# Kernel tuning notes

Hardware: AMD Instinct MI355X
Metric: run time of the kernel (lower is better)

The kernel has to match this reference:

```python
import jax, jax.numpy as jnp
import numpy as np

N_SITES = 100000
DIM = 128
KSIZE = 7  # 7^3 = 343 offsets
GRID = 160


def _build_sparse_structure(seed=0):
    """Sample N_SITES unique voxels in a GRID^3 volume and build the
    depthwise-conv kernel map: neighbor_idx[i, k] = index of site at
    coords[i] + offset[k], or N_SITES (sentinel -> zero row) if absent."""
    rng = np.random.default_rng(seed)
    lin = rng.choice(GRID ** 3, size=N_SITES, replace=False)
    coords = np.stack(np.unravel_index(lin, (GRID, GRID, GRID)), axis=1).astype(np.int64)  # [N,3]
    lookup = np.full(GRID ** 3, N_SITES, dtype=np.int32)
    lookup[lin] = np.arange(N_SITES, dtype=np.int32)
    r = KSIZE // 2
    offs = np.stack(np.meshgrid(*([np.arange(-r, r + 1)] * 3), indexing="ij"), axis=-1).reshape(-1, 3)  # [343,3]
    K = offs.shape[0]
    neighbor_idx = np.full((N_SITES, K), N_SITES, dtype=np.int32)
    for k in range(K):
        nb = coords + offs[k]
        ok = np.all((nb >= 0) & (nb < GRID), axis=1)
        nb_lin = (nb[ok, 0] * GRID + nb[ok, 1]) * GRID + nb[ok, 2]
        neighbor_idx[ok, k] = lookup[nb_lin]
    return neighbor_idx


def setup_inputs() -> dict:
    key = jax.random.key(0)
    ks = jax.random.split(key, 12)
    neighbor_idx = jnp.asarray(_build_sparse_structure(0))
    d, h = DIM, 4 * DIM
    K = KSIZE ** 3
    return {
        "feats": jax.random.normal(ks[0], (N_SITES, d), jnp.float32),
        "neighbor_idx": neighbor_idx,
        "dw_w": jax.random.normal(ks[1], (K, d), jnp.float32) * 0.05,
        "dw_b": jax.random.normal(ks[2], (d,), jnp.float32) * 0.02,
        "ln_g": 1.0 + 0.1 * jax.random.normal(ks[3], (d,), jnp.float32),
        "ln_b": 0.02 * jax.random.normal(ks[4], (d,), jnp.float32),
        "w1": jax.random.normal(ks[5], (d, h), jnp.float32) * (1.0 / np.sqrt(d)),
        "b1": 0.02 * jax.random.normal(ks[6], (h,), jnp.float32),
        "grn_g": 0.1 * jax.random.normal(ks[7], (1, h), jnp.float32),
        "grn_b": 0.02 * jax.random.normal(ks[8], (1, h), jnp.float32),
        "w2": jax.random.normal(ks[9], (h, d), jnp.float32) * (1.0 / np.sqrt(h)),
        "b2": 0.02 * jax.random.normal(ks[10], (d,), jnp.float32),
    }


def reference(feats, neighbor_idx, dw_w, dw_b, ln_g, ln_b, w1, b1, grn_g, grn_b, w2, b2):
    eps = 1e-6
    n, d = feats.shape
    # --- sparse depthwise conv: gather-multiply-accumulate over kernel offsets ---
    f_pad = jnp.concatenate([feats, jnp.zeros((1, d), feats.dtype)], axis=0)  # sentinel row

    def step(acc, xs):
        idx_k, w_k = xs  # idx_k: [N], w_k: [dim]
        return acc + f_pad[idx_k] * w_k, None

    x, _ = jax.lax.scan(step, jnp.zeros_like(feats), (neighbor_idx.T, dw_w))
    x = x + dw_b
    # --- LayerNorm over channels ---
    mu = jnp.mean(x, axis=-1, keepdims=True)
    var = jnp.var(x, axis=-1, keepdims=True)
    x = (x - mu) / jnp.sqrt(var + eps) * ln_g + ln_b
    # --- pwconv1 -> GELU (exact, matching torch default) ---
    x = jax.nn.gelu(x @ w1 + b1, approximate=False)  # [N, 4*dim]
    # --- GRN: L2 norm over all sites (dim=0), per channel ---
    gx = jnp.sqrt(jnp.sum(x * x, axis=0, keepdims=True))  # [1, 4*dim]
    nx = gx / (jnp.mean(gx, axis=-1, keepdims=True) + eps)
    x = grn_g * (x * nx) + grn_b + x
    # --- pwconv2 + residual (drop_path identity in eval) ---
    x = x @ w2 + b2
    return feats + x
```

## Files before the change

### kernel.cpp

```cpp
#include <hip/hip_runtime.h>

typedef unsigned short u16;
typedef unsigned int u32;
typedef __attribute__((ext_vector_type(8))) short bf16x8;
typedef __attribute__((ext_vector_type(4))) float f32x4;

__device__ __forceinline__ u16 f2bf(float f) {
    u32 u = __float_as_uint(f);
    return (u16)((u + 0x7FFFu + ((u >> 16) & 1u)) >> 16);
}

__device__ __forceinline__ float fast_gelu(float x) {
    const float x3 = x * x * x;
    const float y2 = 1.5957691216057308f * (x + 0.044715f * x3);
    const float u = __expf(fminf(y2, 80.f));
    const float th = (u - 1.f) / (u + 1.f);
    return 0.5f * x * (1.f + th);
}

__global__ __launch_bounds__(256) void cast_feats_k(
    const float* __restrict__ src, u16* __restrict__ dst, int n4)
{
    const int e = blockIdx.x * 256 + threadIdx.x;
    if (e >= n4) return;
    const float4 v = *(const float4*)(src + (size_t)e * 4);
    uint2 o;
    o.x = (u32)f2bf(v.x) | ((u32)f2bf(v.y) << 16);
    o.y = (u32)f2bf(v.z) | ((u32)f2bf(v.w) << 16);
    *(uint2*)(dst + (size_t)e * 4) = o;
}

__global__ __launch_bounds__(256) void dwln_k(
    const u16* __restrict__ featsb, const int* __restrict__ nb,
    const u16* __restrict__ dwwb, const float* __restrict__ dw_b,
    const float* __restrict__ ln_g, const float* __restrict__ ln_b,
    u16* __restrict__ xln, int nsites)
{
    __shared__ int lists[8][348];
    const int w = threadIdx.x >> 6;
    const int lane = threadIdx.x & 63;
    const int s0 = blockIdx.x * 8 + w * 2;
    if (s0 >= nsites) return;
    const bool two = (s0 + 1) < nsites;
    const int* rowA = nb + (size_t)s0 * 343;
    const int* rowB = nb + (size_t)(two ? s0 + 1 : s0) * 343;
    int idxA[6], idxB[6];
    #pragma unroll
    for (int j = 0; j < 5; ++j) {
        idxA[j] = rowA[lane + j * 64];
        const int vb = rowB[lane + j * 64];
        idxB[j] = two ? vb : nsites;
    }
    idxA[5] = (lane < 23) ? rowA[320 + lane] : nsites;
    idxB[5] = (two && lane < 23) ? rowB[320 + lane] : nsites;
    int cA = 0, cB = 0;
    #pragma unroll
    for (int i = 0; i < 6; ++i) {
        cA += (idxA[i] < nsites) ? 1 : 0;
        cB += (idxB[i] < nsites) ? 1 : 0;
    }
    const int packed = cA | (cB << 16);
    int pre = packed;
    #pragma unroll
    for (int off = 1; off < 64; off <<= 1) {
        const int v = __shfl_up(pre, off, 64);
        if (lane >= off) pre += v;
    }
    const int tot = __shfl(pre, 63, 64);
    const int cntA = tot & 0xFFFF, cntB = tot >> 16;
    pre -= packed;
    int pA = pre & 0xFFFF, pB = pre >> 16;
    #pragma unroll
    for (int i = 0; i < 6; ++i) {
        const int k = (i < 5) ? (lane + i * 64) : (320 + lane);
        if (idxA[i] < nsites) lists[w * 2][pA++] = idxA[i] | (k << 17);
        if (idxB[i] < nsites) lists[w * 2 + 1][pB++] = idxB[i] | (k << 17);
    }
    float xA0 = 0.f, xA1 = 0.f, xB0 = 0.f, xB1 = 0.f;
    const int mx = (cntA > cntB) ? cntA : cntB;
    for (int base = 0; base < mx; base += 4) {
        u32 fa[4], wa[4], fb[4], wb[4];
        #pragma unroll
        for (int i = 0; i < 4; ++i) {
            if (base + i < cntA) {
                const int p = lists[w * 2][base + i];
                fa[i] = *(const u32*)(featsb + (size_t)(p & 0x1FFFF) * 128 + lane * 2);
                wa[i] = *(const u32*)(dwwb + (size_t)(p >> 17) * 128 + lane * 2);
            } else { fa[i] = 0u; wa[i] = 0u; }
            if (base + i < cntB) {
                const int p = lists[w * 2 + 1][base + i];
                fb[i] = *(const u32*)(featsb + (size_t)(p & 0x1FFFF) * 128 + lane * 2);
                wb[i] = *(const u32*)(dwwb + (size_t)(p >> 17) * 128 + lane * 2);
            } else { fb[i] = 0u; wb[i] = 0u; }
        }
        #pragma unroll
        for (int i = 0; i < 4; ++i) {
            xA0 += __uint_as_float(fa[i] << 16) * __uint_as_float(wa[i] << 16);
            xA1 += __uint_as_float(fa[i] & 0xFFFF0000u) * __uint_as_float(wa[i] & 0xFFFF0000u);
            xB0 += __uint_as_float(fb[i] << 16) * __uint_as_float(wb[i] << 16);
            xB1 += __uint_as_float(fb[i] & 0xFFFF0000u) * __uint_as_float(wb[i] & 0xFFFF0000u);
        }
    }
    const float2 bv = *(const float2*)(dw_b + lane * 2);
    const float2 gv = *(const float2*)(ln_g + lane * 2);
    const float2 lbv = *(const float2*)(ln_b + lane * 2);
    #pragma unroll
    for (int sidx = 0; sidx < 2; ++sidx) {
        if (sidx == 1 && !two) break;
        float a0 = (sidx == 0) ? xA0 : xB0;
        float a1 = (sidx == 0) ? xA1 : xB1;
        a0 += bv.x; a1 += bv.y;
        float s = a0 + a1, ss = a0 * a0 + a1 * a1;
        #pragma unroll
        for (int off = 32; off > 0; off >>= 1) {
            s += __shfl_xor(s, off, 64);
            ss += __shfl_xor(ss, off, 64);
        }
        const float mean = s * (1.f / 128.f);
        const float var = ss * (1.f / 128.f) - mean * mean;
        const float rstd = rsqrtf(fmaxf(var, 0.f) + 1e-6f);
        const float y0 = (a0 - mean) * rstd * gv.x + lbv.x;
        const float y1 = (a1 - mean) * rstd * gv.y + lbv.y;
        *(u32*)(xln + (size_t)(s0 + sidx) * 128 + lane * 2) =
            (u32)f2bf(y0) | ((u32)f2bf(y1) << 16);
    }
}

__global__ __launch_bounds__(256) void transpose_w1_k(
    const float* __restrict__ w1, u16* __restrict__ w1t)
{
    const int e = blockIdx.x * 256 + threadIdx.x;
    const int n = e >> 7, k = e & 127;
    w1t[e] = f2bf(w1[k * 512 + n]);
}

__global__ __launch_bounds__(256, 4) void gemm1_k(
    const u16* __restrict__ xln, const u16* __restrict__ w1t,
    const float* __restrict__ b1, u16* __restrict__ h,
    float* __restrict__ gx_sq, int nsites)
{
    __shared__ float s_red[128];
    const int t = threadIdx.x;
    const int n0 = blockIdx.x * 128;
    const int m0 = blockIdx.y * 64;
    const int lane = t & 63;
    const int w = t >> 6;
    const int wn = w * 32;
    const int l15 = lane & 15, quad = lane >> 4;
    if (t < 128) s_red[t] = 0.f;
    __syncthreads();
    f32x4 acc[2][4];
    #pragma unroll
    for (int i = 0; i < 2; ++i)
        #pragma unroll
        for (int j = 0; j < 4; ++j) acc[i][j] = f32x4{0.f, 0.f, 0.f, 0.f};
    const u16* a_base = w1t + (size_t)(n0 + wn + l15) * 128 + quad * 8;
    const u16* b_base = xln + (size_t)(m0 + l15) * 128 + quad * 8;
    bf16x8 aC[2], bC[4], aN[2], bN[4];
    #pragma unroll
    for (int nt = 0; nt < 2; ++nt) aC[nt] = *(const bf16x8*)(a_base + (size_t)nt * 16 * 128);
    #pragma unroll
    for (int mt = 0; mt < 4; ++mt) bC[mt] = *(const bf16x8*)(b_base + (size_t)mt * 16 * 128);
    #pragma unroll
    for (int ks = 0; ks < 4; ++ks) {
        if (ks < 3) {
            const int koff = (ks + 1) * 32;
            #pragma unroll
            for (int nt = 0; nt < 2; ++nt)
                aN[nt] = *(const bf16x8*)(a_base + (size_t)nt * 16 * 128 + koff);
            #pragma unroll
            for (int mt = 0; mt < 4; ++mt)
                bN[mt] = *(const bf16x8*)(b_base + (size_t)mt * 16 * 128 + koff);
        }
        #pragma unroll
        for (int nt = 0; nt < 2; ++nt)
            #pragma unroll
            for (int mt = 0; mt < 4; ++mt)
                acc[nt][mt] = __builtin_amdgcn_mfma_f32_16x16x32_bf16(aC[nt], bC[mt], acc[nt][mt], 0, 0, 0);
        if (ks < 3) {
            #pragma unroll
            for (int nt = 0; nt < 2; ++nt) aC[nt] = aN[nt];
            #pragma unroll
            for (int mt = 0; mt < 4; ++mt) bC[mt] = bN[mt];
        }
    }
    float ssl[2][4] = {{0.f,0.f,0.f,0.f},{0.f,0.f,0.f,0.f}};
    #pragma unroll
    for (int nt = 0; nt < 2; ++nt) {
        const int chb = n0 + wn + nt * 16 + quad * 4;
        const float4 b1v = *(const float4*)(b1 + chb);
        #pragma unroll
        for (int mt = 0; mt < 4; ++mt) {
            const int site = m0 + mt * 16 + l15;
            if (site < nsites) {
                float v[4];
                #pragma unroll
                for (int rg = 0; rg < 4; ++rg) {
                    v[rg] = fast_gelu(acc[nt][mt][rg] + ((const float*)&b1v)[rg]);
                    ssl[nt][rg] += v[rg] * v[rg];
                }
                uint2 o;
                o.x = (u32)f2bf(v[0]) | ((u32)f2bf(v[1]) << 16);
                o.y = (u32)f2bf(v[2]) | ((u32)f2bf(v[3]) << 16);
                *(uint2*)(h + (size_t)site * 512 + chb) = o;
            }
        }
    }
    #pragma unroll
    for (int nt = 0; nt < 2; ++nt)
        #pragma unroll
        for (int rg = 0; rg < 4; ++rg) {
            float v = ssl[nt][rg];
            v += __shfl_xor(v, 1, 64);
            v += __shfl_xor(v, 2, 64);
            v += __shfl_xor(v, 4, 64);
            v += __shfl_xor(v, 8, 64);
            if (l15 == 0) atomicAdd(&s_red[wn + nt * 16 + quad * 4 + rg], v);
        }
    __syncthreads();
    if (t < 128) atomicAdd(&gx_sq[n0 + t], s_red[t]);
}

__global__ __launch_bounds__(256) void beff_k(
    const float* __restrict__ grn_b, const float* __restrict__ w2,
    float* __restrict__ b_eff)
{
    __shared__ float red[256];
    const int t = threadIdx.x;
    const int dc = t & 127, part = t >> 7;
    const int c0 = blockIdx.x * 64 + part * 32;
    float p = 0.f;
    #pragma unroll 8
    for (int i = 0; i < 32; ++i) {
        const int c = c0 + i;
        p += grn_b[c] * w2[(size_t)c * 128 + dc];
    }
    red[t] = p;
    __syncthreads();
    if (t < 128) atomicAdd(&b_eff[t], red[t] + red[t + 128]);
}

__global__ __launch_bounds__(512) void grn_scale_k(
    const float* __restrict__ gx_sq, const float* __restrict__ grn_g,
    float* __restrict__ scale)
{
    __shared__ float red[512];
    const int t = threadIdx.x;
    const float g = sqrtf(gx_sq[t]);
    red[t] = g;
    __syncthreads();
    #pragma unroll
    for (int off = 256; off > 0; off >>= 1) {
        if (t < off) red[t] += red[t + off];
        __syncthreads();
    }
    const float mean = red[0] * (1.f / 512.f);
    scale[t] = grn_g[t] * (g / (mean + 1e-6f)) + 1.f;
}

__global__ __launch_bounds__(256) void w2t_k(
    const float* __restrict__ scale, const float* __restrict__ w2,
    u16* __restrict__ w2t)
{
    const int e = blockIdx.x * 256 + threadIdx.x;
    const int c = e & 511, dc = e >> 9;
    w2t[e] = f2bf(scale[c] * w2[(size_t)c * 128 + dc]);
}

__global__ __launch_bounds__(256, 4) void gemm2_k(
    const u16* __restrict__ h, const u16* __restrict__ w2t,
    const float* __restrict__ b_eff, const float* __restrict__ b2,
    const float* __restrict__ feats,
    float* __restrict__ out, int nsites)
{
    const int t = threadIdx.x;
    const int m0 = blockIdx.x * 64;
    const int lane = t & 63;
    const int w = t >> 6;
    const int wn = w * 32;
    const int l15 = lane & 15, quad = lane >> 4;
    f32x4 acc[2][4];
    #pragma unroll
    for (int i = 0; i < 2; ++i)
        #pragma unroll
        for (int j = 0; j < 4; ++j) acc[i][j] = f32x4{0.f, 0.f, 0.f, 0.f};
    const u16* a_base = w2t + (size_t)(wn + l15) * 512 + quad * 8;
    const u16* b_base = h + (size_t)(m0 + l15) * 512 + quad * 8;
    bf16x8 aC[2], bC[4], aN[2], bN[4];
    #pragma unroll
    for (int nt = 0; nt < 2; ++nt) aC[nt] = *(const bf16x8*)(a_base + (size_t)nt * 16 * 512);
    #pragma unroll
    for (int mt = 0; mt < 4; ++mt) bC[mt] = *(const bf16x8*)(b_base + (size_t)mt * 16 * 512);
    #pragma unroll
    for (int ks = 0; ks < 16; ++ks) {
        if (ks < 15) {
            const int koff = (ks + 1) * 32;
            #pragma unroll
            for (int nt = 0; nt < 2; ++nt)
                aN[nt] = *(const bf16x8*)(a_base + (size_t)nt * 16 * 512 + koff);
            #pragma unroll
            for (int mt = 0; mt < 4; ++mt)
                bN[mt] = *(const bf16x8*)(b_base + (size_t)mt * 16 * 512 + koff);
        }
        #pragma unroll
        for (int nt = 0; nt < 2; ++nt)
            #pragma unroll
            for (int mt = 0; mt < 4; ++mt)
                acc[nt][mt] = __builtin_amdgcn_mfma_f32_16x16x32_bf16(aC[nt], bC[mt], acc[nt][mt], 0, 0, 0);
        if (ks < 15) {
            #pragma unroll
            for (int nt = 0; nt < 2; ++nt) aC[nt] = aN[nt];
            #pragma unroll
            for (int mt = 0; mt < 4; ++mt) bC[mt] = bN[mt];
        }
    }
    #pragma unroll
    for (int nt = 0; nt < 2; ++nt) {
        const int chb = wn + nt * 16 + quad * 4;
        const float4 bev = *(const float4*)(b_eff + chb);
        const float4 b2v = *(const float4*)(b2 + chb);
        #pragma unroll
        for (int mt = 0; mt < 4; ++mt) {
            const int site = m0 + mt * 16 + l15;
            if (site < nsites) {
                const float4 fv = *(const float4*)(feats + (size_t)site * 128 + chb);
                float4 o;
                o.x = acc[nt][mt][0] + bev.x + b2v.x + fv.x;
                o.y = acc[nt][mt][1] + bev.y + b2v.y + fv.y;
                o.z = acc[nt][mt][2] + bev.z + b2v.z + fv.z;
                o.w = acc[nt][mt][3] + bev.w + b2v.w + fv.w;
                *(float4*)(out + (size_t)site * 128 + chb) = o;
            }
        }
    }
}

extern "C" void kernel_launch(void* const* d_in, const int* in_sizes, int n_in,
                              void* d_out, int out_size, void* d_ws, size_t ws_size,
                              hipStream_t stream) {
    const float* feats = (const float*)d_in[0];
    const int* nb      = (const int*)d_in[1];
    const float* dw_w  = (const float*)d_in[2];
    const float* dw_b  = (const float*)d_in[3];
    const float* ln_g  = (const float*)d_in[4];
    const float* ln_b  = (const float*)d_in[5];
    const float* w1    = (const float*)d_in[6];
    const float* b1    = (const float*)d_in[7];
    const float* grn_g = (const float*)d_in[8];
    const float* grn_b = (const float*)d_in[9];
    const float* w2    = (const float*)d_in[10];
    const float* b2    = (const float*)d_in[11];
    float* out = (float*)d_out;
    const int nsites = in_sizes[0] / 128;

    char* ws = (char*)d_ws;
    size_t off = 0;
    u16* xln   = (u16*)(ws + off);  off += (((size_t)(nsites + 128) * 128 * 2) + 255) & ~(size_t)255;
    u16* h     = (u16*)(ws + off);  off += (((size_t)(nsites + 128) * 512 * 2) + 255) & ~(size_t)255;
    u16* featsb= (u16*)(ws + off);  off += (((size_t)nsites * 128 * 2) + 255) & ~(size_t)255;
    u16* dwwb  = (u16*)(ws + off);  off += 343 * 128 * 2 + 128;
    u16* w1t   = (u16*)(ws + off);  off += 512 * 128 * 2;
    u16* w2t   = (u16*)(ws + off);  off += 128 * 512 * 2;
    float* gx_sq = (float*)(ws + off); off += 512 * 4;
    float* scale = (float*)(ws + off); off += 512 * 4;
    float* b_eff = (float*)(ws + off); off += 128 * 4;

    hipMemsetAsync(gx_sq, 0, 512 * sizeof(float), stream);
    hipMemsetAsync(b_eff, 0, 128 * sizeof(float), stream);
    const int nfeat4 = nsites * 32;
    cast_feats_k<<<(nfeat4 + 255) / 256, 256, 0, stream>>>(feats, featsb, nfeat4);
    const int ndww4 = 343 * 32;
    cast_feats_k<<<(ndww4 + 255) / 256, 256, 0, stream>>>(dw_w, dwwb, ndww4);
    transpose_w1_k<<<256, 256, 0, stream>>>(w1, w1t);
    beff_k<<<8, 256, 0, stream>>>(grn_b, w2, b_eff);
    dwln_k<<<(nsites + 7) / 8, 256, 0, stream>>>(featsb, nb, dwwb, dw_b, ln_g, ln_b, xln, nsites);
    const int m1blocks = (nsites + 63) / 64;
    gemm1_k<<<dim3(4, m1blocks), 256, 0, stream>>>(xln, w1t, b1, h, gx_sq, nsites);
    grn_scale_k<<<1, 512, 0, stream>>>(gx_sq, grn_g, scale);
    w2t_k<<<256, 256, 0, stream>>>(scale, w2, w2t);
    const int m2blocks = (nsites + 63) / 64;
    gemm2_k<<<m2blocks, 256, 0, stream>>>(h, w2t, b_eff, b2, feats, out, nsites);
}
```

Before: 473.2 us.

## Stage activation tiles in swizzled LDS via direct global-to-LDS loads in both GEMMs

In gemm1 and gemm2, each wave used to load the activation (B) operand straight from global memory, so all four waves fetched the same rows redundantly. The activation tile is now copied once per block into XOR-swizzled shared memory using global_load_lds, and gemm2 double-buffers it across K chunks. GELU is also rewritten in the algebraically equivalent sigmoid form x*u/(u+1) with a hardware reciprocal. This cuts redundant global and L2 traffic, at the cost of LDS usage, which may lower occupancy, and extra barriers. The gemm1 tile load has no bounds check on the last partial block.

```diff
diff --git a/kernel.cpp b/kernel.cpp
--- a/kernel.cpp
+++ b/kernel.cpp
@@ -11,11 +11,16 @@
 }
 
 __device__ __forceinline__ float fast_gelu(float x) {
-    const float x3 = x * x * x;
-    const float y2 = 1.5957691216057308f * (x + 0.044715f * x3);
+    const float t = x * x;
+    const float y2 = x * __builtin_fmaf(0.0713548214f, t, 1.5957691216057308f);
     const float u = __expf(fminf(y2, 80.f));
-    const float th = (u - 1.f) / (u + 1.f);
-    return 0.5f * x * (1.f + th);
+    return x * u * __builtin_amdgcn_rcpf(u + 1.f);
+}
+
+__device__ __forceinline__ void gload_lds16(const u16* g, u16* l) {
+    __builtin_amdgcn_global_load_lds(
+        (const __attribute__((address_space(1))) void*)g,
+        (__attribute__((address_space(3))) void*)l, 16, 0, 0);
 }
 
 __global__ __launch_bounds__(256) void cast_feats_k(
@@ -139,6 +144,7 @@
     const float* __restrict__ b1, u16* __restrict__ h,
     float* __restrict__ gx_sq, int nsites)
 {
+    __shared__ u16 xb[64 * 128];
     __shared__ float s_red[128];
     const int t = threadIdx.x;
     const int n0 = blockIdx.x * 128;
@@ -148,40 +154,46 @@
     const int wn = w * 32;
     const int l15 = lane & 15, quad = lane >> 4;
     if (t < 128) s_red[t] = 0.f;
-    __syncthreads();
+    #pragma unroll
+    for (int i = 0; i < 4; ++i) {
+        const int r = w * 16 + i * 4 + (lane >> 4);
+        const int c = (lane & 15) ^ (r & 15);
+        gload_lds16(xln + (size_t)(m0 + r) * 128 + c * 8,
+                    &xb[(w * 16 + i * 4) * 128]);
+    }
     f32x4 acc[2][4];
     #pragma unroll
     for (int i = 0; i < 2; ++i)
         #pragma unroll
         for (int j = 0; j < 4; ++j) acc[i][j] = f32x4{0.f, 0.f, 0.f, 0.f};
     const u16* a_base = w1t + (size_t)(n0 + wn + l15) * 128 + quad * 8;
-    const u16* b_base = xln + (size_t)(m0 + l15) * 128 + quad * 8;
-    bf16x8 aC[2], bC[4], aN[2], bN[4];
+    bf16x8 aC[2];
     #pragma unroll
     for (int nt = 0; nt < 2; ++nt) aC[nt] = *(const bf16x8*)(a_base + (size_t)nt * 16 * 128);
-    #pragma unroll
-    for (int mt = 0; mt < 4; ++mt) bC[mt] = *(const bf16x8*)(b_base + (size_t)mt * 16 * 128);
+    asm volatile("s_waitcnt vmcnt(0)" ::: "memory");
+    __syncthreads();
     #pragma unroll
     for (int ks = 0; ks < 4; ++ks) {
+        bf16x8 aN[2];
         if (ks < 3) {
-            const int koff = (ks + 1) * 32;
             #pragma unroll
             for (int nt = 0; nt < 2; ++nt)
-                aN[nt] = *(const bf16x8*)(a_base + (size_t)nt * 16 * 128 + koff);
-            #pragma unroll
-            for (int mt = 0; mt < 4; ++mt)
-                bN[mt] = *(const bf16x8*)(b_base + (size_t)mt * 16 * 128 + koff);
+                aN[nt] = *(const bf16x8*)(a_base + (size_t)nt * 16 * 128 + (ks + 1) * 32);
+        }
+        bf16x8 b[4];
+        #pragma unroll
+        for (int mt = 0; mt < 4; ++mt) {
+            const int r = mt * 16 + l15;
+            b[mt] = *(const bf16x8*)(&xb[r * 128 + (((ks * 4 + quad) ^ l15) << 3)]);
         }
         #pragma unroll
         for (int nt = 0; nt < 2; ++nt)
             #pragma unroll
             for (int mt = 0; mt < 4; ++mt)
-                acc[nt][mt] = __builtin_amdgcn_mfma_f32_16x16x32_bf16(aC[nt], bC[mt], acc[nt][mt], 0, 0, 0);
+                acc[nt][mt] = __builtin_amdgcn_mfma_f32_16x16x32_bf16(aC[nt], b[mt], acc[nt][mt], 0, 0, 0);
         if (ks < 3) {
             #pragma unroll
             for (int nt = 0; nt < 2; ++nt) aC[nt] = aN[nt];
-            #pragma unroll
-            for (int mt = 0; mt < 4; ++mt) bC[mt] = bN[mt];
         }
     }
     float ssl[2][4] = {{0.f,0.f,0.f,0.f},{0.f,0.f,0.f,0.f}};
@@ -273,47 +285,73 @@
     const float* __restrict__ feats,
     float* __restrict__ out, int nsites)
 {
+    __shared__ u16 hb[2][64 * 128];
     const int t = threadIdx.x;
     const int m0 = blockIdx.x * 64;
     const int lane = t & 63;
     const int w = t >> 6;
     const int wn = w * 32;
     const int l15 = lane & 15, quad = lane >> 4;
+    const int r_st = w * 16 + (lane >> 4) * 4 ? 0 : 0;
     f32x4 acc[2][4];
     #pragma unroll
     for (int i = 0; i < 2; ++i)
         #pragma unroll
         for (int j = 0; j < 4; ++j) acc[i][j] = f32x4{0.f, 0.f, 0.f, 0.f};
     const u16* a_base = w2t + (size_t)(wn + l15) * 512 + quad * 8;
-    const u16* b_base = h + (size_t)(m0 + l15) * 512 + quad * 8;
-    bf16x8 aC[2], bC[4], aN[2], bN[4];
+
+    #define STAGE2(bsel, tc)                                                     \
+        {                                                                        \
+            _Pragma("unroll")                                                    \
+            for (int i_ = 0; i_ < 4; ++i_) {                                     \
+                const int r_ = w * 16 + i_ * 4 + (lane >> 4);                    \
+                const int c_ = (lane & 15) ^ (r_ & 15);                          \
+                gload_lds16(h + (size_t)(m0 + r_) * 512 + (tc) * 128 + c_ * 8,   \
+                            &hb[bsel][(w * 16 + i_ * 4) * 128]);                 \
+            }                                                                    \
+        }
+
+    STAGE2(0, 0)
+    bf16x8 aC[2];
     #pragma unroll
     for (int nt = 0; nt < 2; ++nt) aC[nt] = *(const bf16x8*)(a_base + (size_t)nt * 16 * 512);
-    #pragma unroll
-    for (int mt = 0; mt < 4; ++mt) bC[mt] = *(const bf16x8*)(b_base + (size_t)mt * 16 * 512);
-    #pragma unroll
-    for (int ks = 0; ks < 16; ++ks) {
-        if (ks < 15) {
-            const int koff = (ks + 1) * 32;
+    asm volatile("s_waitcnt vmcnt(0)" ::: "memory");
+    __syncthreads();
+    #pragma unroll
+    for (int tch = 0; tch < 4; ++tch) {
+        const int cur = tch & 1;
+        if (tch < 3) STAGE2(cur ^ 1, tch + 1)
+        #pragma unroll
+        for (int ks = 0; ks < 4; ++ks) {
+            const int ksg = tch * 4 + ks;
+            bf16x8 aN[2];
+            if (ksg < 15) {
+                #pragma unroll
+                for (int nt = 0; nt < 2; ++nt)
+                    aN[nt] = *(const bf16x8*)(a_base + (size_t)nt * 16 * 512 + (ksg + 1) * 32);
+            }
+            bf16x8 b[4];
+            #pragma unroll
+            for (int mt = 0; mt < 4; ++mt) {
+                const int r = mt * 16 + l15;
+                b[mt] = *(const bf16x8*)(&hb[cur][r * 128 + (((ks * 4 + quad) ^ l15) << 3)]);
+            }
             #pragma unroll
             for (int nt = 0; nt < 2; ++nt)
-                aN[nt] = *(const bf16x8*)(a_base + (size_t)nt * 16 * 512 + koff);
-            #pragma unroll
-            for (int mt = 0; mt < 4; ++mt)
-                bN[mt] = *(const bf16x8*)(b_base + (size_t)mt * 16 * 512 + koff);
-        }
-        #pragma unroll
-        for (int nt = 0; nt < 2; ++nt)
-            #pragma unroll
-            for (int mt = 0; mt < 4; ++mt)
-                acc[nt][mt] = __builtin_amdgcn_mfma_f32_16x16x32_bf16(aC[nt], bC[mt], acc[nt][mt], 0, 0, 0);
-        if (ks < 15) {
-            #pragma unroll
-            for (int nt = 0; nt < 2; ++nt) aC[nt] = aN[nt];
-            #pragma unroll
-            for (int mt = 0; mt < 4; ++mt) bC[mt] = bN[mt];
-        }
-    }
+                #pragma unroll
+                for (int mt = 0; mt < 4; ++mt)
+                    acc[nt][mt] = __builtin_amdgcn_mfma_f32_16x16x32_bf16(aC[nt], b[mt], acc[nt][mt], 0, 0, 0);
+            if (ksg < 15) {
+                #pragma unroll
+                for (int nt = 0; nt < 2; ++nt) aC[nt] = aN[nt];
+            }
+        }
+        if (tch < 3) {
+            asm volatile("s_waitcnt vmcnt(0)" ::: "memory");
+            __syncthreads();
+        }
+    }
+    #undef STAGE2
     #pragma unroll
     for (int nt = 0; nt < 2; ++nt) {
         const int chb = wn + nt * 16 + quad * 4;
```

Measured after the change: 411.0 us. 13.1% less time.
